# Optimization experiments

Measured on AMD Instinct MI355X. Metric: run time of the kernel, lower is better.

## Reference

```python
import jax, jax.numpy as jnp
import numpy as np

L, D = 2048, 1024
D_INNER = 2 * D          # expand=2
D_STATE = 16
D_CONV = 4
DT_RANK = D // 16        # ceil(1024/16) = 64
HID = 4 * D
EPS = 1e-5


def _layernorm(x, g, b):
    mu = jnp.mean(x, axis=-1, keepdims=True)
    var = jnp.mean(jnp.square(x - mu), axis=-1, keepdims=True)
    return (x - mu) * jax.lax.rsqrt(var + EPS) * g + b


def setup_inputs() -> dict:
    key = jax.random.key(0)
    ks = jax.random.split(key, 12)
    f = lambda k, sh, s=0.02: (jax.random.normal(k, sh, jnp.float32) * s)
    return {
        "x": jax.random.normal(ks[0], (L, D), jnp.float32),
        "ln1_g": jnp.ones((D,), jnp.float32),
        "ln1_b": jnp.zeros((D,), jnp.float32),
        "ln2_g": jnp.ones((D,), jnp.float32),
        "ln2_b": jnp.zeros((D,), jnp.float32),
        "in_proj_w": f(ks[1], (2 * D_INNER, D)),
        "conv_w": f(ks[2], (D_INNER, D_CONV), 0.1),
        "conv_b": jnp.zeros((D_INNER,), jnp.float32),
        "x_proj_w": f(ks[3], (DT_RANK + 2 * D_STATE, D_INNER)),
        "dt_proj_w": f(ks[4], (D_INNER, DT_RANK), 0.1),
        "dt_proj_b": f(ks[5], (D_INNER,), 0.1),
        "A_log": jnp.log(jnp.broadcast_to(
            jnp.arange(1, D_STATE + 1, dtype=jnp.float32), (D_INNER, D_STATE))),
        "D_param": jnp.ones((D_INNER,), jnp.float32),
        "out_proj_w": f(ks[6], (D, D_INNER)),
        "ffn_w1": f(ks[7], (HID, D)),
        "ffn_b1": jnp.zeros((HID,), jnp.float32),
        "ffn_w2": f(ks[8], (D, HID)),
        "ffn_b2": jnp.zeros((D,), jnp.float32),
    }


def _mamba(x, in_proj_w, conv_w, conv_b, x_proj_w, dt_proj_w, dt_proj_b,
           A_log, D_param, out_proj_w):
    # x: (L, D)
    xz = x @ in_proj_w.T                    # (L, 2*d_inner)
    xm, z = xz[:, :D_INNER], xz[:, D_INNER:]
    # causal depthwise conv1d, kernel d_conv, output length L
    xp = jnp.pad(xm, ((D_CONV - 1, 0), (0, 0)))
    xc = conv_b
    for k in range(D_CONV):                 # 4 taps, fixed small loop
        xc = xc + xp[k:k + L] * conv_w[None, :, k]
    xc = jax.nn.silu(xc)                    # (L, d_inner)
    proj = xc @ x_proj_w.T                  # (L, dt_rank + 2*d_state)
    dt = proj[:, :DT_RANK]
    B = proj[:, DT_RANK:DT_RANK + D_STATE]  # (L, d_state)
    C = proj[:, DT_RANK + D_STATE:]         # (L, d_state)
    delta = jax.nn.softplus(dt @ dt_proj_w.T + dt_proj_b)  # (L, d_inner)
    A = -jnp.exp(A_log)                     # (d_inner, d_state)
    dA = jnp.exp(delta[:, :, None] * A[None])               # (L, d_inner, d_state)
    dBx = delta[:, :, None] * B[:, None, :] * xc[:, :, None]

    def step(h, inp):
        dA_t, dBx_t, C_t = inp
        h = h * dA_t + dBx_t                # (d_inner, d_state)
        y = jnp.einsum('ds,s->d', h, C_t)
        return h, y

    h0 = jnp.zeros((D_INNER, D_STATE), x.dtype)
    _, ys = jax.lax.scan(step, h0, (dA, dBx, C))            # ys: (L, d_inner)
    y = ys + xc * D_param
    y = y * jax.nn.silu(z)
    return y @ out_proj_w.T                 # (L, D)


def reference(x, ln1_g, ln1_b, ln2_g, ln2_b, in_proj_w, conv_w, conv_b,
              x_proj_w, dt_proj_w, dt_proj_b, A_log, D_param, out_proj_w,
              ffn_w1, ffn_b1, ffn_w2, ffn_b2):
    residual = x
    h = _layernorm(x, ln1_g, ln1_b)
    h = _mamba(h, in_proj_w, conv_w, conv_b, x_proj_w, dt_proj_w, dt_proj_b,
               A_log, D_param, out_proj_w)
    h = h + residual
    # FFN has an internal residual around the normed input, plus outer residual
    n = _layernorm(h, ln2_g, ln2_b)
    f = n + (jax.nn.relu(n @ ffn_w1.T + ffn_b1) @ ffn_w2.T + ffn_b2)
    return h + f
```

## Files before the change

### kernel.cpp

```cpp
#include <hip/hip_runtime.h>
#include <hip/hip_bf16.h>
#include <math.h>

#define L_SEQ 2048
#define DMODEL 1024
#define DINNER 2048
#define DSTATE 16
#define DTRANK 64
#define NHID 4096
#define NC 64
#define LC 32

typedef __bf16 bf16_t;
typedef __bf16 bf16x4 __attribute__((ext_vector_type(4)));
typedef __bf16 bf16x8 __attribute__((ext_vector_type(8)));
typedef float f32x4 __attribute__((ext_vector_type(4)));

#define WAIT_VM0 0x0F70
#define WAIT_VM4 0x0F74
#define WAIT_VM8 0x0F78

__device__ __forceinline__ void async_cp16(const bf16_t* g, bf16_t* l) {
    __builtin_amdgcn_global_load_lds(
        (const __attribute__((address_space(1))) void*)g,
        (__attribute__((address_space(3))) void*)l, 16, 0, 0);
}

template <int EPI, int SPLIT>
__global__ __launch_bounds__(512, 4) void gemm_big(
    const bf16_t* __restrict__ A, int lda,
    const bf16_t* __restrict__ W, int ldw,
    bf16_t* __restrict__ C, int ldc,
    int Kslice, long cstride,
    const float* __restrict__ bias)
{
    __shared__ bf16_t As[2 * 8192];
    __shared__ bf16_t Ws[2 * 4096];

    const int tid  = threadIdx.x;
    const int lane = tid & 63;
    const int w    = tid >> 6;

    int my, mx, kz;
    if (SPLIT == 0) {
        int lid = blockIdx.y * 32 + blockIdx.x;
        int r = lid & 7, i = lid >> 3;
        my = (r >> 2) * 4 + (i & 3);
        mx = (r & 3) * 8 + (i >> 2);
        kz = 0;
    } else {
        int id = (blockIdx.z * 8 + blockIdx.y) * 8 + blockIdx.x;
        int r = id & 7, i = id >> 3;
        kz = r >> 1;
        my = i & 7;
        mx = (r & 1) * 4 + (i >> 3);
    }
    const int m0 = my * 256;
    const int n0 = mx * 128;
    const int k0 = kz * Kslice;

    const int p    = lane & 3;
    const int rA0  = 2 * w * 16 + (lane >> 2);
    const int rA1  = rA0 + 16;
    const int rW   = w * 16 + (lane >> 2);
    const int dcA0 = (p - ((rA0 >> 1) & 3)) & 3;
    const int dcA1 = (p - ((rA1 >> 1) & 3)) & 3;
    const int dcW  = (p - ((rW  >> 1) & 3)) & 3;

    const bf16_t* gA0 = A + (size_t)(m0 + rA0) * lda + k0 + dcA0 * 8;
    const bf16_t* gA1 = A + (size_t)(m0 + rA1) * lda + k0 + dcA1 * 8;
    const bf16_t* gW  = W + (size_t)(n0 + rW) * ldw + k0 + dcW * 8;
    const int aLo0 = (2 * w) * 512;
    const int aLo1 = aLo0 + 512;
    const int wLo  = w * 512;

    const int wr   = w >> 1;
    const int wc   = w & 1;
    const int quad = lane >> 4;
    const int lr   = lane & 15;
    int offA[4], offW[4];
    #pragma unroll
    for (int i = 0; i < 4; ++i) {
        int ra = wr * 64 + i * 16 + lr;
        offA[i] = ra * 32 + (((quad + ((ra >> 1) & 3)) & 3) * 8);
        int rb = wc * 64 + i * 16 + lr;
        offW[i] = rb * 32 + (((quad + ((rb >> 1) & 3)) & 3) * 8);
    }

    const int niter = Kslice >> 5;

    async_cp16(gA0, &As[aLo0]);
    async_cp16(gA1, &As[aLo1]);
    async_cp16(gW,  &Ws[wLo]);
    gA0 += 32; gA1 += 32; gW += 32;

    f32x4 acc[4][4] = {};
    for (int it = 0; it < niter; ++it) {
        __builtin_amdgcn_s_waitcnt(WAIT_VM0);
        __builtin_amdgcn_s_barrier();
        asm volatile("" ::: "memory");

        if (it + 1 < niter) {
            int sa = ((it + 1) & 1) * 8192;
            int sw = ((it + 1) & 1) * 4096;
            async_cp16(gA0, &As[sa + aLo0]);
            async_cp16(gA1, &As[sa + aLo1]);
            async_cp16(gW,  &Ws[sw + wLo]);
            gA0 += 32; gA1 += 32; gW += 32;
        }

        const int ca = (it & 1) * 8192;
        const int cw = (it & 1) * 4096;
        bf16x8 af[4], bw[4];
        #pragma unroll
        for (int i = 0; i < 4; ++i) af[i] = *(const bf16x8*)&As[ca + offA[i]];
        #pragma unroll
        for (int j = 0; j < 4; ++j) bw[j] = *(const bf16x8*)&Ws[cw + offW[j]];
        #pragma unroll
        for (int i = 0; i < 4; ++i)
            #pragma unroll
            for (int j = 0; j < 4; ++j)
                acc[i][j] = __builtin_amdgcn_mfma_f32_16x16x32_bf16(af[i], bw[j], acc[i][j], 0, 0, 0);
    }

    bf16_t* Cb = C + (size_t)kz * cstride;
    #pragma unroll
    for (int i = 0; i < 4; ++i) {
        int row0 = m0 + wr * 64 + i * 16 + quad * 4;
        #pragma unroll
        for (int j = 0; j < 4; ++j) {
            int col = n0 + wc * 64 + j * 16 + lr;
            float bv = (EPI == 2) ? bias[col] : 0.f;
            #pragma unroll
            for (int r = 0; r < 4; ++r) {
                float v = acc[i][j][r];
                if (EPI == 2) v = fmaxf(v + bv, 0.f);
                Cb[(size_t)(row0 + r) * ldc + col] = (bf16_t)v;
            }
        }
    }
}

template <int EPI, int OUTBF16>
__global__ __launch_bounds__(256) void gemm_async(
    const bf16_t* __restrict__ A, int lda,
    const bf16_t* __restrict__ W, int ldw,
    void* __restrict__ Cv, int ldc,
    int N, int Kslice, long cstride,
    const float* __restrict__ bias)
{
    __shared__ bf16_t As[4 * 4096];
    __shared__ bf16_t Ws[4 * 4096];

    const int tid  = threadIdx.x;
    const int lane = tid & 63;
    const int w    = tid >> 6;
    const int m0   = blockIdx.y * 128;
    const int n0   = blockIdx.x * 128;
    const int kz   = blockIdx.z;
    const int k0   = kz * Kslice;

    const int p   = lane & 3;
    const int r0  = 2 * w * 16 + (lane >> 2);
    const int r1  = r0 + 16;
    const int dc0 = (p - ((r0 >> 1) & 3)) & 3;
    const int dc1 = (p - ((r1 >> 1) & 3)) & 3;

    const bf16_t* gA0 = A + (size_t)(m0 + r0) * lda + k0 + dc0 * 8;
    const bf16_t* gA1 = A + (size_t)(m0 + r1) * lda + k0 + dc1 * 8;
    int gn0 = n0 + r0; if (gn0 > N - 1) gn0 = N - 1;
    int gn1 = n0 + r1; if (gn1 > N - 1) gn1 = N - 1;
    const bf16_t* gW0 = W + (size_t)gn0 * ldw + k0 + dc0 * 8;
    const bf16_t* gW1 = W + (size_t)gn1 * ldw + k0 + dc1 * 8;

    const int lo0 = (2 * w) * 512;
    const int lo1 = lo0 + 512;

    const int wr   = w >> 1;
    const int wc   = w & 1;
    const int quad = lane >> 4;
    const int lr   = lane & 15;
    int offA[4], offW[4];
    #pragma unroll
    for (int i = 0; i < 4; ++i) {
        int ra = wr * 64 + i * 16 + lr;
        offA[i] = ra * 32 + (((quad + ((ra >> 1) & 3)) & 3) * 8);
        int rb = wc * 64 + i * 16 + lr;
        offW[i] = rb * 32 + (((quad + ((rb >> 1) & 3)) & 3) * 8);
    }

    const int niter = Kslice >> 5;

    #pragma unroll
    for (int j = 0; j < 3; ++j) {
        if (j < niter) {
            int sb = j * 4096;
            async_cp16(gA0, &As[sb + lo0]);
            async_cp16(gA1, &As[sb + lo1]);
            async_cp16(gW0, &Ws[sb + lo0]);
            async_cp16(gW1, &Ws[sb + lo1]);
            gA0 += 32; gA1 += 32; gW0 += 32; gW1 += 32;
        }
    }

    f32x4 acc[4][4] = {};
    for (int it = 0; it < niter; ++it) {
        if (it + 3 <= niter)      __builtin_amdgcn_s_waitcnt(WAIT_VM8);
        else if (it + 2 <= niter) __builtin_amdgcn_s_waitcnt(WAIT_VM4);
        else                      __builtin_amdgcn_s_waitcnt(WAIT_VM0);
        __builtin_amdgcn_s_barrier();
        asm volatile("" ::: "memory");

        if (it + 3 < niter) {
            int sb = ((it + 3) & 3) * 4096;
            async_cp16(gA0, &As[sb + lo0]);
            async_cp16(gA1, &As[sb + lo1]);
            async_cp16(gW0, &Ws[sb + lo0]);
            async_cp16(gW1, &Ws[sb + lo1]);
            gA0 += 32; gA1 += 32; gW0 += 32; gW1 += 32;
        }

        const int cb = (it & 3) * 4096;
        bf16x8 af[4], bw[4];
        #pragma unroll
        for (int i = 0; i < 4; ++i) af[i] = *(const bf16x8*)&As[cb + offA[i]];
        #pragma unroll
        for (int j = 0; j < 4; ++j) bw[j] = *(const bf16x8*)&Ws[cb + offW[j]];
        #pragma unroll
        for (int i = 0; i < 4; ++i)
            #pragma unroll
            for (int j = 0; j < 4; ++j)
                acc[i][j] = __builtin_amdgcn_mfma_f32_16x16x32_bf16(af[i], bw[j], acc[i][j], 0, 0, 0);
    }

    float*  Cf = (float*)Cv + (size_t)kz * cstride;
    bf16_t* Cb = (bf16_t*)Cv + (size_t)kz * cstride;
    #pragma unroll
    for (int i = 0; i < 4; ++i) {
        int row0 = m0 + wr * 64 + i * 16 + quad * 4;
        #pragma unroll
        for (int j = 0; j < 4; ++j) {
            int col = n0 + wc * 64 + j * 16 + lr;
            if (col < N) {
                float bv = (EPI == 3) ? bias[col] : 0.f;
                #pragma unroll
                for (int r = 0; r < 4; ++r) {
                    float v = acc[i][j][r];
                    if (EPI == 3) {
                        float t = v + bv;
                        v = fmaxf(t, 0.f) + log1pf(__expf(-fabsf(t)));
                    }
                    size_t o = (size_t)(row0 + r) * ldc + col;
                    if (OUTBF16) Cb[o] = (bf16_t)v;
                    else         Cf[o] = v;
                }
            }
        }
    }
}

__global__ __launch_bounds__(256) void cvt_ln1(
    const float* __restrict__ s0, const float* __restrict__ s1,
    const float* __restrict__ s2, const float* __restrict__ s3,
    const float* __restrict__ s4, const float* __restrict__ s5,
    bf16_t* __restrict__ dst,
    const float* __restrict__ x, const float* __restrict__ g,
    const float* __restrict__ b, bf16_t* __restrict__ outb)
{
    if (blockIdx.x < 14656) {
        int e = (blockIdx.x * 256 + threadIdx.x) * 4;
        const float* src; int local;
        if      (e < 4194304)  { src = s0; local = e; }
        else if (e < 4390912)  { src = s1; local = e - 4194304; }
        else if (e < 4521984)  { src = s2; local = e - 4390912; }
        else if (e < 6619136)  { src = s3; local = e - 4521984; }
        else if (e < 10813440) { src = s4; local = e - 6619136; }
        else                   { src = s5; local = e - 10813440; }
        float4 v = *(const float4*)(src + local);
        bf16x4 o;
        o[0] = (bf16_t)v.x; o[1] = (bf16_t)v.y; o[2] = (bf16_t)v.z; o[3] = (bf16_t)v.w;
        *(bf16x4*)(dst + e) = o;
        return;
    }
    const int row = blockIdx.x - 14656;
    const float* xr = x + (size_t)row * DMODEL;
    float v[4];
    float s = 0.f, sq = 0.f;
    #pragma unroll
    for (int i = 0; i < 4; ++i) {
        v[i] = xr[threadIdx.x + i * 256];
        s += v[i]; sq += v[i] * v[i];
    }
    #pragma unroll
    for (int off = 32; off > 0; off >>= 1) {
        s += __shfl_xor(s, off); sq += __shfl_xor(sq, off);
    }
    __shared__ float rs_[4], rq_[4];
    int w = threadIdx.x >> 6;
    if ((threadIdx.x & 63) == 0) { rs_[w] = s; rq_[w] = sq; }
    __syncthreads();
    s  = rs_[0] + rs_[1] + rs_[2] + rs_[3];
    sq = rq_[0] + rq_[1] + rq_[2] + rq_[3];
    float mu  = s * (1.f / DMODEL);
    float var = sq * (1.f / DMODEL) - mu * mu;
    float rsd = rsqrtf(var + 1e-5f);
    #pragma unroll
    for (int i = 0; i < 4; ++i) {
        int col = threadIdx.x + i * 256;
        outb[(size_t)row * DMODEL + col] = (bf16_t)((v[i] - mu) * rsd * g[col] + b[col]);
    }
}

__global__ __launch_bounds__(256) void conv_silu(
    const bf16_t* __restrict__ xz, const float* __restrict__ cw,
    const float* __restrict__ cb, bf16_t* __restrict__ xc)
{
    int gid = blockIdx.x * 256 + threadIdx.x;
    int c = gid & (DINNER - 1);
    int t = gid >> 11;
    float acc = cb[c];
    #pragma unroll
    for (int k = 0; k < 4; ++k) {
        int tt = t + k - 3;
        if (tt >= 0) acc += (float)xz[(size_t)tt * (2 * DINNER) + c] * cw[c * 4 + k];
    }
    float sig = 1.f / (1.f + __expf(-acc));
    xc[gid] = (bf16_t)(acc * sig);
}

__global__ __launch_bounds__(256) void scan_pass1(
    const bf16_t* __restrict__ delta, const bf16_t* __restrict__ xc,
    const float* __restrict__ proj, const float* __restrict__ A_log,
    float* __restrict__ carryH, float* __restrict__ sumd)
{
    const int c = blockIdx.x;
    const int d = blockIdx.y * 256 + threadIdx.x;
    const int t0 = c * LC;

    __shared__ float Bs[LC][DSTATE];
    for (int i = threadIdx.x; i < LC * DSTATE; i += 256) {
        int tt = i >> 4, s = i & 15;
        Bs[tt][s] = proj[(size_t)(t0 + tt) * 96 + DTRANK + s];
    }
    __syncthreads();

    float a[DSTATE], h[DSTATE];
    #pragma unroll
    for (int s = 0; s < DSTATE; ++s) {
        a[s] = -__expf(A_log[d * DSTATE + s]);
        h[s] = 0.f;
    }
    float sd = 0.f;
    for (int i = 0; i < LC; ++i) {
        int t = t0 + i;
        float dl = (float)delta[(size_t)t * DINNER + d];
        float x  = (float)xc[(size_t)t * DINNER + d];
        sd += dl;
        float dx = dl * x;
        #pragma unroll
        for (int s = 0; s < DSTATE; ++s)
            h[s] = h[s] * __expf(dl * a[s]) + dx * Bs[i][s];
    }
    #pragma unroll
    for (int s = 0; s < DSTATE; ++s)
        carryH[((size_t)c * DINNER + d) * DSTATE + s] = h[s];
    sumd[c * DINNER + d] = sd;
}

__global__ __launch_bounds__(256) void scan_pass2(
    const float* __restrict__ A_log, const float* __restrict__ carryH,
    const float* __restrict__ sumd, float* __restrict__ hinit)
{
    int idx = blockIdx.x * 256 + threadIdx.x;
    int d = idx >> 4;
    float a = -__expf(A_log[idx]);
    float hc = 0.f;
    for (int c0 = 0; c0 < NC; c0 += 8) {
        float H[8], P[8];
        #pragma unroll
        for (int j = 0; j < 8; ++j) {
            H[j] = carryH[(size_t)(c0 + j) * (DINNER * DSTATE) + idx];
            P[j] = __expf(a * sumd[(c0 + j) * DINNER + d]);
        }
        #pragma unroll
        for (int j = 0; j < 8; ++j) {
            hinit[(size_t)(c0 + j) * (DINNER * DSTATE) + idx] = hc;
            hc = H[j] + P[j] * hc;
        }
    }
}

__global__ __launch_bounds__(256) void scan_pass3(
    const bf16_t* __restrict__ delta, const bf16_t* __restrict__ xc,
    const float* __restrict__ proj, const float* __restrict__ A_log,
    const float* __restrict__ hinit, const float* __restrict__ Dp,
    const bf16_t* __restrict__ xz, bf16_t* __restrict__ yact)
{
    const int c = blockIdx.x;
    const int d = blockIdx.y * 256 + threadIdx.x;
    const int t0 = c * LC;

    __shared__ float Bs[LC][DSTATE], Cs[LC][DSTATE];
    for (int i = threadIdx.x; i < LC * DSTATE; i += 256) {
        int tt = i >> 4, s = i & 15;
        size_t base = (size_t)(t0 + tt) * 96;
        Bs[tt][s] = proj[base + DTRANK + s];
        Cs[tt][s] = proj[base + DTRANK + DSTATE + s];
    }
    __syncthreads();

    float a[DSTATE], h[DSTATE];
    #pragma unroll
    for (int s = 0; s < DSTATE; ++s) {
        a[s] = -__expf(A_log[d * DSTATE + s]);
        h[s] = hinit[(size_t)c * (DINNER * DSTATE) + d * DSTATE + s];
    }
    float DD = Dp[d];
    for (int i = 0; i < LC; ++i) {
        int t = t0 + i;
        float dl = (float)delta[(size_t)t * DINNER + d];
        float x  = (float)xc[(size_t)t * DINNER + d];
        float dx = dl * x;
        float y = 0.f;
        #pragma unroll
        for (int s = 0; s < DSTATE; ++s) {
            h[s] = h[s] * __expf(dl * a[s]) + dx * Bs[i][s];
            y += h[s] * Cs[i][s];
        }
        float yv = y + x * DD;
        float z = (float)xz[(size_t)t * (2 * DINNER) + DINNER + d];
        float sil = z / (1.f + __expf(-z));
        yact[(size_t)t * DINNER + d] = (bf16_t)(yv * sil);
    }
}

__global__ __launch_bounds__(256) void reduce4(
    const float* __restrict__ part, float* __restrict__ proj,
    bf16_t* __restrict__ projdt)
{
    int i = blockIdx.x * 256 + threadIdx.x;
    float v = 0.f;
    #pragma unroll
    for (int s = 0; s < 16; ++s) v += part[(size_t)s * 196608 + i];
    proj[i] = v;
    int row = i / 96;
    int col = i - row * 96;
    if (col < DTRANK) projdt[row * DTRANK + col] = (bf16_t)v;
}

__global__ __launch_bounds__(256) void red9_ln2(
    const bf16_t* __restrict__ part, const float* __restrict__ x,
    const float* __restrict__ g, const float* __restrict__ b,
    float* __restrict__ hres, float* __restrict__ nbuf,
    bf16_t* __restrict__ nbufb)
{
    const int row = blockIdx.x;
    const size_t base = (size_t)row * DMODEL;
    float v[4];
    float s = 0.f, sq = 0.f;
    #pragma unroll
    for (int i = 0; i < 4; ++i) {
        int col = threadIdx.x + i * 256;
        float acc = x[base + col];
        #pragma unroll
        for (int sl = 0; sl < 4; ++sl)
            acc += (float)part[(size_t)sl * 2097152 + base + col];
        hres[base + col] = acc;
        v[i] = acc; s += acc; sq += acc * acc;
    }
    #pragma unroll
    for (int off = 32; off > 0; off >>= 1) {
        s += __shfl_xor(s, off); sq += __shfl_xor(sq, off);
    }
    __shared__ float rs_[4], rq_[4];
    int w = threadIdx.x >> 6;
    if ((threadIdx.x & 63) == 0) { rs_[w] = s; rq_[w] = sq; }
    __syncthreads();
    s  = rs_[0] + rs_[1] + rs_[2] + rs_[3];
    sq = rq_[0] + rq_[1] + rq_[2] + rq_[3];
    float mu  = s * (1.f / DMODEL);
    float var = sq * (1.f / DMODEL) - mu * mu;
    float rsd = rsqrtf(var + 1e-5f);
    #pragma unroll
    for (int i = 0; i < 4; ++i) {
        int col = threadIdx.x + i * 256;
        float o = (v[i] - mu) * rsd * g[col] + b[col];
        nbuf[base + col] = o;
        nbufb[base + col] = (bf16_t)o;
    }
}

__global__ __launch_bounds__(256) void reduce12(
    const bf16_t* __restrict__ part, const float* __restrict__ b2,
    const float* __restrict__ hres, const float* __restrict__ nbuf,
    float* __restrict__ out)
{
    int i = (blockIdx.x * 256 + threadIdx.x) * 4;
    float4 bb = *(const float4*)(b2 + (i & (DMODEL - 1)));
    float4 h  = *(const float4*)(hres + i);
    float4 n  = *(const float4*)(nbuf + i);
    float s0 = bb.x + h.x + n.x, s1 = bb.y + h.y + n.y;
    float s2 = bb.z + h.z + n.z, s3 = bb.w + h.w + n.w;
    #pragma unroll
    for (int sl = 0; sl < 4; ++sl) {
        bf16x4 v = *(const bf16x4*)(part + (size_t)sl * 2097152 + i);
        s0 += (float)v[0]; s1 += (float)v[1]; s2 += (float)v[2]; s3 += (float)v[3];
    }
    *(float4*)(out + i) = make_float4(s0, s1, s2, s3);
}

extern "C" void kernel_launch(void* const* d_in, const int* in_sizes, int n_in,
                              void* d_out, int out_size, void* d_ws, size_t ws_size,
                              hipStream_t stream)
{
    const float* x        = (const float*)d_in[0];
    const float* ln1_g    = (const float*)d_in[1];
    const float* ln1_b    = (const float*)d_in[2];
    const float* ln2_g    = (const float*)d_in[3];
    const float* ln2_b    = (const float*)d_in[4];
    const float* in_proj  = (const float*)d_in[5];
    const float* conv_w   = (const float*)d_in[6];
    const float* conv_b   = (const float*)d_in[7];
    const float* x_proj   = (const float*)d_in[8];
    const float* dt_proj  = (const float*)d_in[9];
    const float* dt_b     = (const float*)d_in[10];
    const float* A_log    = (const float*)d_in[11];
    const float* D_param  = (const float*)d_in[12];
    const float* out_proj = (const float*)d_in[13];
    const float* ffn_w1   = (const float*)d_in[14];
    const float* ffn_b1   = (const float*)d_in[15];
    const float* ffn_w2   = (const float*)d_in[16];
    const float* ffn_b2   = (const float*)d_in[17];
    float* out = (float*)d_out;

    char* base = (char*)d_ws;
    bf16_t* Wb     = (bf16_t*)(base);
    bf16_t* w_inp  = Wb;
    bf16_t* w_xp   = Wb + 4194304;
    bf16_t* w_dtp  = Wb + 4390912;
    bf16_t* w_outp = Wb + 4521984;
    bf16_t* w_f1   = Wb + 6619136;
    bf16_t* w_f2   = Wb + 10813440;

    bf16_t* h1b    = (bf16_t*)(base + 30015488);
    float*  proj   = (float*)(base + 30015488);
    bf16_t* projdt = (bf16_t*)(base + 30015488 + 786432);
    bf16_t* xz     = (bf16_t*)(base + 34209792);
    bf16_t* ffnh   = xz;
    bf16_t* xc     = (bf16_t*)(base + 50987008);
    float*  part   = (float*)(base + 59375616);
    bf16_t* delta  = (bf16_t*)part;
    bf16_t* partb  = (bf16_t*)part;
    float*  carry  = (float*)(base + 76152832);
    bf16_t* nbufb  = (bf16_t*)carry;
    float*  sumd   = (float*)(base + 84541440);
    float*  hinit  = (float*)(base + 85065728);
    float*  nbuf   = hinit;
    bf16_t* yact   = (bf16_t*)(base + 93454336);
    float*  hres   = (float*)(base + 101842944);

    cvt_ln1<<<14656 + 2048, 256, 0, stream>>>(in_proj, x_proj, dt_proj, out_proj,
                                              ffn_w1, ffn_w2, Wb,
                                              x, ln1_g, ln1_b, h1b);
    gemm_big<0, 0><<<dim3(32, 8), 512, 0, stream>>>(
        h1b, DMODEL, w_inp, DMODEL, xz, 4096, 1024, 0, nullptr);
    conv_silu<<<(L_SEQ * DINNER) / 256, 256, 0, stream>>>(xz, conv_w, conv_b, xc);
    gemm_async<0, 0><<<dim3(1, 16, 16), 256, 0, stream>>>(
        xc, DINNER, w_xp, DINNER, part, 96, 96, 128, 196608L, nullptr);
    reduce4<<<768, 256, 0, stream>>>(part, proj, projdt);
    gemm_async<3, 1><<<dim3(16, 16, 1), 256, 0, stream>>>(
        projdt, DTRANK, w_dtp, DTRANK, delta, DINNER, DINNER, DTRANK, 0, dt_b);
    scan_pass1<<<dim3(NC, DINNER / 256), 256, 0, stream>>>(delta, xc, proj, A_log, carry, sumd);
    scan_pass2<<<(DINNER * DSTATE) / 256, 256, 0, stream>>>(A_log, carry, sumd, hinit);
    scan_pass3<<<dim3(NC, DINNER / 256), 256, 0, stream>>>(delta, xc, proj, A_log, hinit,
                                                           D_param, xz, yact);
    gemm_big<0, 1><<<dim3(8, 8, 4), 512, 0, stream>>>(
        yact, DINNER, w_outp, DINNER, partb, DMODEL, 512, 2097152L, nullptr);
    red9_ln2<<<L_SEQ, 256, 0, stream>>>(partb, x, ln2_g, ln2_b, hres, nbuf, nbufb);
    gemm_big<2, 0><<<dim3(32, 8), 512, 0, stream>>>(
        nbufb, DMODEL, w_f1, DMODEL, ffnh, NHID, 1024, 0, ffn_b1);
    gemm_big<0, 1><<<dim3(8, 8, 4), 512, 0, stream>>>(
        ffnh, NHID, w_f2, NHID, partb, DMODEL, 1024, 2097152L, nullptr);
    reduce12<<<2048, 256, 0, stream>>>(partb, ffn_b2, hres, nbuf, out);
}
```

Measured before the change: 417.3 us.

## Replace async-pipelined small GEMM with padded-LDS simple GEMM and prefetch scan inputs

The small GEMMs (x_proj and dt_proj) drop the 4-stage async global-to-LDS pipeline in favour of a plain synchronous load into padded shared tiles with K-steps of 64. These GEMMs have short K (128 and 64), so pipeline prologue and waitcnt overhead may dominate. The scan passes 1 and 3 software-prefetch the next timestep's delta, xc and z into registers to hide global load latency behind the recurrence. Risks are the loss of load/compute overlap in the GEMM and some extra register pressure in the scans.

```diff
diff --git a/kernel.cpp b/kernel.cpp
--- a/kernel.cpp
+++ b/kernel.cpp
@@ -17,8 +17,6 @@
 typedef float f32x4 __attribute__((ext_vector_type(4)));
 
 #define WAIT_VM0 0x0F70
-#define WAIT_VM4 0x0F74
-#define WAIT_VM8 0x0F78
 
 __device__ __forceinline__ void async_cp16(const bf16_t* g, bf16_t* l) {
     __builtin_amdgcn_global_load_lds(
@@ -142,15 +140,15 @@
 }
 
 template <int EPI, int OUTBF16>
-__global__ __launch_bounds__(256) void gemm_async(
+__global__ __launch_bounds__(256) void gemm_simple(
     const bf16_t* __restrict__ A, int lda,
     const bf16_t* __restrict__ W, int ldw,
     void* __restrict__ Cv, int ldc,
     int N, int Kslice, long cstride,
     const float* __restrict__ bias)
 {
-    __shared__ bf16_t As[4 * 4096];
-    __shared__ bf16_t Ws[4 * 4096];
+    __shared__ bf16_t As[128 * 72];
+    __shared__ bf16_t Ws[128 * 72];
 
     const int tid  = threadIdx.x;
     const int lane = tid & 63;
@@ -160,77 +158,43 @@
     const int kz   = blockIdx.z;
     const int k0   = kz * Kslice;
 
-    const int p   = lane & 3;
-    const int r0  = 2 * w * 16 + (lane >> 2);
-    const int r1  = r0 + 16;
-    const int dc0 = (p - ((r0 >> 1) & 3)) & 3;
-    const int dc1 = (p - ((r1 >> 1) & 3)) & 3;
-
-    const bf16_t* gA0 = A + (size_t)(m0 + r0) * lda + k0 + dc0 * 8;
-    const bf16_t* gA1 = A + (size_t)(m0 + r1) * lda + k0 + dc1 * 8;
-    int gn0 = n0 + r0; if (gn0 > N - 1) gn0 = N - 1;
-    int gn1 = n0 + r1; if (gn1 > N - 1) gn1 = N - 1;
-    const bf16_t* gW0 = W + (size_t)gn0 * ldw + k0 + dc0 * 8;
-    const bf16_t* gW1 = W + (size_t)gn1 * ldw + k0 + dc1 * 8;
-
-    const int lo0 = (2 * w) * 512;
-    const int lo1 = lo0 + 512;
-
     const int wr   = w >> 1;
     const int wc   = w & 1;
     const int quad = lane >> 4;
     const int lr   = lane & 15;
-    int offA[4], offW[4];
-    #pragma unroll
-    for (int i = 0; i < 4; ++i) {
-        int ra = wr * 64 + i * 16 + lr;
-        offA[i] = ra * 32 + (((quad + ((ra >> 1) & 3)) & 3) * 8);
-        int rb = wc * 64 + i * 16 + lr;
-        offW[i] = rb * 32 + (((quad + ((rb >> 1) & 3)) & 3) * 8);
-    }
-
-    const int niter = Kslice >> 5;
-
-    #pragma unroll
-    for (int j = 0; j < 3; ++j) {
-        if (j < niter) {
-            int sb = j * 4096;
-            async_cp16(gA0, &As[sb + lo0]);
-            async_cp16(gA1, &As[sb + lo1]);
-            async_cp16(gW0, &Ws[sb + lo0]);
-            async_cp16(gW1, &Ws[sb + lo1]);
-            gA0 += 32; gA1 += 32; gW0 += 32; gW1 += 32;
-        }
-    }
 
     f32x4 acc[4][4] = {};
-    for (int it = 0; it < niter; ++it) {
-        if (it + 3 <= niter)      __builtin_amdgcn_s_waitcnt(WAIT_VM8);
-        else if (it + 2 <= niter) __builtin_amdgcn_s_waitcnt(WAIT_VM4);
-        else                      __builtin_amdgcn_s_waitcnt(WAIT_VM0);
-        __builtin_amdgcn_s_barrier();
-        asm volatile("" ::: "memory");
-
-        if (it + 3 < niter) {
-            int sb = ((it + 3) & 3) * 4096;
-            async_cp16(gA0, &As[sb + lo0]);
-            async_cp16(gA1, &As[sb + lo1]);
-            async_cp16(gW0, &Ws[sb + lo0]);
-            async_cp16(gW1, &Ws[sb + lo1]);
-            gA0 += 32; gA1 += 32; gW0 += 32; gW1 += 32;
-        }
-
-        const int cb = (it & 3) * 4096;
-        bf16x8 af[4], bw[4];
-        #pragma unroll
-        for (int i = 0; i < 4; ++i) af[i] = *(const bf16x8*)&As[cb + offA[i]];
-        #pragma unroll
-        for (int j = 0; j < 4; ++j) bw[j] = *(const bf16x8*)&Ws[cb + offW[j]];
-        #pragma unroll
-        for (int i = 0; i < 4; ++i)
+
+    for (int k = 0; k < Kslice; k += 64) {
+        __syncthreads();
+        #pragma unroll
+        for (int i = 0; i < 4; ++i) {
+            int idx = tid + i * 256;
+            int row = idx >> 3;
+            int c8  = (idx & 7) * 8;
+            *(bf16x8*)&As[row * 72 + c8] =
+                *(const bf16x8*)(A + (size_t)(m0 + row) * lda + k0 + k + c8);
+            int gn = n0 + row; if (gn > N - 1) gn = N - 1;
+            *(bf16x8*)&Ws[row * 72 + c8] =
+                *(const bf16x8*)(W + (size_t)gn * ldw + k0 + k + c8);
+        }
+        __syncthreads();
+
+        #pragma unroll
+        for (int kk = 0; kk < 64; kk += 32) {
+            bf16x8 af[4], bw[4];
+            #pragma unroll
+            for (int i = 0; i < 4; ++i)
+                af[i] = *(const bf16x8*)&As[(wr * 64 + i * 16 + lr) * 72 + kk + quad * 8];
             #pragma unroll
             for (int j = 0; j < 4; ++j)
-                acc[i][j] = __builtin_amdgcn_mfma_f32_16x16x32_bf16(af[i], bw[j], acc[i][j], 0, 0, 0);
+                bw[j] = *(const bf16x8*)&Ws[(wc * 64 + j * 16 + lr) * 72 + kk + quad * 8];
+            #pragma unroll
+            for (int i = 0; i < 4; ++i)
+                #pragma unroll
+                for (int j = 0; j < 4; ++j)
+                    acc[i][j] = __builtin_amdgcn_mfma_f32_16x16x32_bf16(af[i], bw[j], acc[i][j], 0, 0, 0);
+        }
     }
 
     float*  Cf = (float*)Cv + (size_t)kz * cstride;
@@ -351,15 +315,20 @@
         h[s] = 0.f;
     }
     float sd = 0.f;
+    float dl = (float)delta[(size_t)t0 * DINNER + d];
+    float x  = (float)xc[(size_t)t0 * DINNER + d];
     for (int i = 0; i < LC; ++i) {
-        int t = t0 + i;
-        float dl = (float)delta[(size_t)t * DINNER + d];
-        float x  = (float)xc[(size_t)t * DINNER + d];
+        float dln = 0.f, xn = 0.f;
+        if (i + 1 < LC) {
+            dln = (float)delta[(size_t)(t0 + i + 1) * DINNER + d];
+            xn  = (float)xc[(size_t)(t0 + i + 1) * DINNER + d];
+        }
         sd += dl;
         float dx = dl * x;
         #pragma unroll
         for (int s = 0; s < DSTATE; ++s)
             h[s] = h[s] * __expf(dl * a[s]) + dx * Bs[i][s];
+        dl = dln; x = xn;
     }
     #pragma unroll
     for (int s = 0; s < DSTATE; ++s)
@@ -416,10 +385,17 @@
         h[s] = hinit[(size_t)c * (DINNER * DSTATE) + d * DSTATE + s];
     }
     float DD = Dp[d];
+    float dl = (float)delta[(size_t)t0 * DINNER + d];
+    float x  = (float)xc[(size_t)t0 * DINNER + d];
+    float z  = (float)xz[(size_t)t0 * (2 * DINNER) + DINNER + d];
     for (int i = 0; i < LC; ++i) {
-        int t = t0 + i;
-        float dl = (float)delta[(size_t)t * DINNER + d];
-        float x  = (float)xc[(size_t)t * DINNER + d];
+        float dln = 0.f, xn = 0.f, zn = 0.f;
+        if (i + 1 < LC) {
+            int tn = t0 + i + 1;
+            dln = (float)delta[(size_t)tn * DINNER + d];
+            xn  = (float)xc[(size_t)tn * DINNER + d];
+            zn  = (float)xz[(size_t)tn * (2 * DINNER) + DINNER + d];
+        }
         float dx = dl * x;
         float y = 0.f;
         #pragma unroll
@@ -428,9 +404,9 @@
             y += h[s] * Cs[i][s];
         }
         float yv = y + x * DD;
-        float z = (float)xz[(size_t)t * (2 * DINNER) + DINNER + d];
         float sil = z / (1.f + __expf(-z));
-        yact[(size_t)t * DINNER + d] = (bf16_t)(yv * sil);
+        yact[(size_t)(t0 + i) * DINNER + d] = (bf16_t)(yv * sil);
+        dl = dln; x = xn; z = zn;
     }
 }
 
@@ -565,10 +541,10 @@
     gemm_big<0, 0><<<dim3(32, 8), 512, 0, stream>>>(
         h1b, DMODEL, w_inp, DMODEL, xz, 4096, 1024, 0, nullptr);
     conv_silu<<<(L_SEQ * DINNER) / 256, 256, 0, stream>>>(xz, conv_w, conv_b, xc);
-    gemm_async<0, 0><<<dim3(1, 16, 16), 256, 0, stream>>>(
+    gemm_simple<0, 0><<<dim3(1, 16, 16), 256, 0, stream>>>(
         xc, DINNER, w_xp, DINNER, part, 96, 96, 128, 196608L, nullptr);
     reduce4<<<768, 256, 0, stream>>>(part, proj, projdt);
-    gemm_async<3, 1><<<dim3(16, 16, 1), 256, 0, stream>>>(
+    gemm_simple<3, 1><<<dim3(16, 16, 1), 256, 0, stream>>>(
         projdt, DTRANK, w_dtp, DTRANK, delta, DINNER, DINNER, DTRANK, 0, dt_b);
     scan_pass1<<<dim3(NC, DINNER / 256), 256, 0, stream>>>(delta, xc, proj, A_log, carry, sumd);
     scan_pass2<<<(DINNER * DSTATE) / 256, 256, 0, stream>>>(A_log, carry, sumd, hinit);
```

After: 403.0 us. 3.4% less time.
